# Optimization experiments

Measured on AMD Instinct MI355X. Metric: run time of the kernel, lower is better.

## Reference

```python
import jax, jax.numpy as jnp
import numpy as np

INPUT_SIZE = 300
HIDDEN = 16


def setup_inputs() -> dict:
    key = jax.random.key(0)
    ks = jax.random.split(key, 9)
    T, B = 512, 512
    s_ih = 1.0 / np.sqrt(HIDDEN)
    inp = {
        "x": jax.random.normal(ks[0], (T, B, INPUT_SIZE), dtype=jnp.float32),
        # LSTMCell params (torch gate order: i, f, g, o)
        "W_ih": jax.random.uniform(ks[1], (4 * HIDDEN, INPUT_SIZE), jnp.float32, -s_ih, s_ih),
        "W_hh": jax.random.uniform(ks[2], (4 * HIDDEN, HIDDEN), jnp.float32, -s_ih, s_ih),
        "b_ih": jax.random.uniform(ks[3], (4 * HIDDEN,), jnp.float32, -s_ih, s_ih),
        "b_hh": jax.random.uniform(ks[4], (4 * HIDDEN,), jnp.float32, -s_ih, s_ih),
        # MLP head
        "W1": jax.random.uniform(ks[5], (64, HIDDEN), jnp.float32, -s_ih, s_ih),
        "b1": jax.random.uniform(ks[6], (64,), jnp.float32, -s_ih, s_ih),
        "W2": jax.random.uniform(ks[7], (1, 64), jnp.float32, -0.125, 0.125),
        "b2": jax.random.uniform(ks[8], (1,), jnp.float32, -0.125, 0.125),
    }
    return inp


def _lstm_final_h(x, W_ih, W_hh, b_ih, b_hh):
    B = x.shape[1]
    h0 = jnp.zeros((B, HIDDEN), dtype=x.dtype)
    c0 = jnp.zeros((B, HIDDEN), dtype=x.dtype)
    # precompute input projections for all timesteps: [T, B, 4H]
    xg = jnp.einsum("tbi,gi->tbg", x, W_ih) + b_ih + b_hh

    def step(carry, xg_t):
        h, c = carry
        gates = xg_t + h @ W_hh.T  # [B, 4H]
        i, f, g, o = jnp.split(gates, 4, axis=-1)
        c = jax.nn.sigmoid(f) * c + jax.nn.sigmoid(i) * jnp.tanh(g)
        h = jax.nn.sigmoid(o) * jnp.tanh(c)
        return (h, c), None

    (h, _), _ = jax.lax.scan(step, (h0, c0), xg)
    return h  # [B, HIDDEN]


def reference(x, W_ih, W_hh, b_ih, b_hh, W1, b1, W2, b2):
    h = _lstm_final_h(x, W_ih, W_hh, b_ih, b_hh)
    # eval mode: dropout is identity
    z = jax.nn.relu(h @ W1.T + b1)
    out = 4.0 * jax.nn.sigmoid(z @ W2.T + b2)
    return out.squeeze(-1)  # [B]
```

## Files before the change

kernel.cpp:

```cpp
#include <hip/hip_runtime.h>
#include <hip/hip_bf16.h>


#define T_STEPS 512
#define BATCH   512
#define K_IN    300
#define NG      64
#define HID     16
#define DPF     8

typedef float  f32x2  __attribute__((ext_vector_type(2)));
typedef float  f32x4  __attribute__((ext_vector_type(4)));
typedef float  f32x8  __attribute__((ext_vector_type(8)));
typedef __bf16 bf16x8 __attribute__((ext_vector_type(8)));

static __device__ __forceinline__ bf16x8 cvt8(float4 lo, float4 hi) {
    f32x8 t;
    t[0] = lo.x; t[1] = lo.y; t[2] = lo.z; t[3] = lo.w;
    t[4] = hi.x; t[5] = hi.y; t[6] = hi.z; t[7] = hi.w;
    return __builtin_convertvector(t, bf16x8);
}

__global__ __launch_bounds__(256) void xg_gemm(
    const float* __restrict__ x,
    const float* __restrict__ W,
    const float* __restrict__ b_ih,
    const float* __restrict__ b_hh,
    float* __restrict__ xg)
{
    __shared__ __align__(16) __bf16 Wl[40 * 512];

    const int lane = threadIdx.x & 63;
    const int wv   = threadIdx.x >> 6;
    const int m16  = lane & 15;
    const int quad = lane >> 4;
    const int row0 = blockIdx.x * 64 + wv * 16;
    const float4 z4 = {0.f, 0.f, 0.f, 0.f};

    const float* xr = x + (size_t)(row0 + m16) * K_IN;

    float4 alo[10], ahi[10];
#pragma unroll
    for (int ks = 0; ks < 10; ++ks) {
        const int k = ks * 32 + quad * 8;
        alo[ks] = (k + 3 < K_IN) ? *(const float4*)(xr + k)     : z4;
        ahi[ks] = (k + 7 < K_IN) ? *(const float4*)(xr + k + 4) : z4;
    }

    {
        const float* wrow = W + (size_t)(wv * 16 + m16) * K_IN;
#pragma unroll
        for (int ks = 0; ks < 10; ++ks) {
            const int k = ks * 32 + quad * 8;
            const float4 lo = (k + 3 < K_IN) ? *(const float4*)(wrow + k)     : z4;
            const float4 hi = (k + 7 < K_IN) ? *(const float4*)(wrow + k + 4) : z4;
            *(bf16x8*)&Wl[(ks * 4 + wv) * 512 + lane * 8] = cvt8(lo, hi);
        }
    }
    __syncthreads();

    f32x4 acc[4];
#pragma unroll
    for (int nt = 0; nt < 4; ++nt) acc[nt] = (f32x4){0.f, 0.f, 0.f, 0.f};

#pragma unroll
    for (int ks = 0; ks < 10; ++ks) {
        const bf16x8 af = cvt8(alo[ks], ahi[ks]);
#pragma unroll
        for (int nt = 0; nt < 4; ++nt) {
            const bf16x8 bf = *(const bf16x8*)&Wl[(ks * 4 + nt) * 512 + lane * 8];
            acc[nt] = __builtin_amdgcn_mfma_f32_16x16x32_bf16(af, bf, acc[nt], 0, 0, 0);
        }
    }

    float bias[4];
#pragma unroll
    for (int nt = 0; nt < 4; ++nt)
        bias[nt] = b_ih[nt * 16 + m16] + b_hh[nt * 16 + m16];

#pragma unroll
    for (int reg = 0; reg < 4; ++reg) {
        const int R = row0 + quad * 4 + reg;
        const int t = R >> 9;
        const int b = R & (BATCH - 1);
        float4 o;
        o.x = acc[0][reg] + bias[0];
        o.y = acc[1][reg] + bias[1];
        o.z = acc[2][reg] + bias[2];
        o.w = acc[3][reg] + bias[3];
        *(float4*)(xg + ((size_t)b * T_STEPS + t) * NG + m16 * 4) = o;
    }
}

__global__ __launch_bounds__(64) void lstm_scan(
    const float* __restrict__ xg,
    const float* __restrict__ Whh,
    const float* __restrict__ W1,
    const float* __restrict__ b1,
    const float* __restrict__ W2,
    const float* __restrict__ b2,
    float* __restrict__ out)
{
    const int lane = threadIdx.x;
    const int q = lane >> 4;
    const int j = lane & 15;
    const int batch = blockIdx.x * 4 + q;
    const int pbase = (lane & 48) << 2;

    f32x2 wi2[8], wf2[8], wg2[8], wo2[8];
#pragma unroll
    for (int k4 = 0; k4 < 4; ++k4) {
        float4 a;
        a = *(const float4*)(Whh + (j     ) * HID + k4 * 4);
        wi2[k4 * 2] = (f32x2){a.x, a.y}; wi2[k4 * 2 + 1] = (f32x2){a.z, a.w};
        a = *(const float4*)(Whh + (j + 16) * HID + k4 * 4);
        wf2[k4 * 2] = (f32x2){a.x, a.y}; wf2[k4 * 2 + 1] = (f32x2){a.z, a.w};
        a = *(const float4*)(Whh + (j + 32) * HID + k4 * 4);
        wg2[k4 * 2] = (f32x2){a.x, a.y}; wg2[k4 * 2 + 1] = (f32x2){a.z, a.w};
        a = *(const float4*)(Whh + (j + 48) * HID + k4 * 4);
        wo2[k4 * 2] = (f32x2){a.x, a.y}; wo2[k4 * 2 + 1] = (f32x2){a.z, a.w};
    }

    float c = 0.f;
    f32x2 hb2[8];
#pragma unroll
    for (int k = 0; k < 8; ++k) hb2[k] = (f32x2){0.f, 0.f};

    const float* xgb = xg + (size_t)batch * T_STEPS * NG + j * 4;

    float4 ring[DPF];
#pragma unroll
    for (int u = 0; u < DPF; ++u)
        ring[u] = *(const float4*)(xgb + (size_t)u * NG);

#pragma unroll 1
    for (int tt = 0; tt < T_STEPS; tt += DPF) {
#pragma unroll
        for (int u = 0; u < DPF; ++u) {
            const int t = tt + u;
            const float4 v = ring[u];
            int tl = t + DPF; if (tl > T_STEPS - 1) tl = T_STEPS - 1;
            ring[u] = *(const float4*)(xgb + (size_t)tl * NG);

            f32x2 si2 = (f32x2){v.x, 0.f};
            f32x2 sf2 = (f32x2){v.y, 0.f};
            f32x2 sg2 = (f32x2){v.z, 0.f};
            f32x2 so2 = (f32x2){v.w, 0.f};
#pragma unroll
            for (int k = 0; k < 8; ++k) {
                si2 += wi2[k] * hb2[k];
                sf2 += wf2[k] * hb2[k];
                sg2 += wg2[k] * hb2[k];
                so2 += wo2[k] * hb2[k];
            }
            const float si = si2[0] + si2[1];
            const float sf = sf2[0] + sf2[1];
            const float sg = sg2[0] + sg2[1];
            const float so = so2[0] + so2[1];

            const float ai = __builtin_amdgcn_rcpf(1.f + __expf(-si));
            const float af = __builtin_amdgcn_rcpf(1.f + __expf(-sf));
            const float ao = __builtin_amdgcn_rcpf(1.f + __expf(-so));
            const float tg = fmaf(2.f, __builtin_amdgcn_rcpf(1.f + __expf(-2.f * sg)), -1.f);

            c = fmaf(af, c, ai * tg);
            const float th = fmaf(2.f, __builtin_amdgcn_rcpf(1.f + __expf(-2.f * c)), -1.f);
            const float h = ao * th;

            const int hI = __float_as_int(h);
#pragma unroll
            for (int k = 0; k < HID; ++k)
                hb2[k >> 1][k & 1] =
                    __int_as_float(__builtin_amdgcn_ds_bpermute(pbase + 4 * k, hI));
        }
    }

    float y = 0.f;
#pragma unroll
    for (int u4 = 0; u4 < 4; ++u4) {
        const int u = u4 * 16 + j;
        float z = b1[u];
#pragma unroll
        for (int k = 0; k < HID; ++k)
            z = fmaf(W1[u * HID + k], hb2[k >> 1][k & 1], z);
        z = fmaxf(z, 0.f);
        y = fmaf(z, W2[u], y);
    }
#pragma unroll
    for (int m = 8; m; m >>= 1) y += __shfl_xor(y, m, 64);

    if (j == 0)
        out[batch] = 4.f * __builtin_amdgcn_rcpf(1.f + __expf(-(y + b2[0])));
}

extern "C" void kernel_launch(void* const* d_in, const int* in_sizes, int n_in,
                              void* d_out, int out_size, void* d_ws, size_t ws_size,
                              hipStream_t stream) {
    const float* x    = (const float*)d_in[0];
    const float* W_ih = (const float*)d_in[1];
    const float* W_hh = (const float*)d_in[2];
    const float* b_ih = (const float*)d_in[3];
    const float* b_hh = (const float*)d_in[4];
    const float* W1   = (const float*)d_in[5];
    const float* b1   = (const float*)d_in[6];
    const float* W2   = (const float*)d_in[7];
    const float* b2   = (const float*)d_in[8];
    float* out = (float*)d_out;
    float* xg  = (float*)d_ws;

    xg_gemm<<<dim3(T_STEPS * BATCH / 64), dim3(256), 0, stream>>>(x, W_ih, b_ih, b_hh, xg);
    lstm_scan<<<dim3(BATCH / 4), dim3(64), 0, stream>>>(xg, W_hh, W1, b1, W2, b2, out);
}
```

Before: 566.5 us.

## Map one batch per wavefront with one gate per lane in LSTM scan

```diff
diff --git a/kernel.cpp b/kernel.cpp
--- a/kernel.cpp
+++ b/kernel.cpp
@@ -7,9 +7,8 @@
 #define K_IN    300
 #define NG      64
 #define HID     16
-#define DPF     8
-
-typedef float  f32x2  __attribute__((ext_vector_type(2)));
+#define CHUNK   16
+
 typedef float  f32x4  __attribute__((ext_vector_type(4)));
 typedef float  f32x8  __attribute__((ext_vector_type(8)));
 typedef __bf16 bf16x8 __attribute__((ext_vector_type(8)));
@@ -101,95 +100,105 @@
     const float* __restrict__ b2,
     float* __restrict__ out)
 {
-    const int lane = threadIdx.x;
-    const int q = lane >> 4;
-    const int j = lane & 15;
-    const int batch = blockIdx.x * 4 + q;
-    const int pbase = (lane & 48) << 2;
-
-    f32x2 wi2[8], wf2[8], wg2[8], wo2[8];
-#pragma unroll
-    for (int k4 = 0; k4 < 4; ++k4) {
-        float4 a;
-        a = *(const float4*)(Whh + (j     ) * HID + k4 * 4);
-        wi2[k4 * 2] = (f32x2){a.x, a.y}; wi2[k4 * 2 + 1] = (f32x2){a.z, a.w};
-        a = *(const float4*)(Whh + (j + 16) * HID + k4 * 4);
-        wf2[k4 * 2] = (f32x2){a.x, a.y}; wf2[k4 * 2 + 1] = (f32x2){a.z, a.w};
-        a = *(const float4*)(Whh + (j + 32) * HID + k4 * 4);
-        wg2[k4 * 2] = (f32x2){a.x, a.y}; wg2[k4 * 2 + 1] = (f32x2){a.z, a.w};
-        a = *(const float4*)(Whh + (j + 48) * HID + k4 * 4);
-        wo2[k4 * 2] = (f32x2){a.x, a.y}; wo2[k4 * 2 + 1] = (f32x2){a.z, a.w};
-    }
+    __shared__ __align__(16) float xs[2][CHUNK][NG];
+
+    const int lane  = threadIdx.x;
+    const int j     = lane & 15;
+    const int qd    = lane >> 4;
+    const int batch = blockIdx.x;
+    const int perm  = j * 4 + qd;
+
+    float w[HID];
+#pragma unroll
+    for (int k = 0; k < HID; k += 4)
+        *(float4*)&w[k] = *(const float4*)(Whh + lane * HID + k);
+
+    const float kk = (qd == 2) ? -2.f : -1.f;
+    const float mm = (qd == 2) ?  2.f :  1.f;
+    const float nn = (qd == 2) ? -1.f :  0.f;
+
+    const int aI = 4 * j, aF = 4 * (16 + j), aG = 4 * (32 + j), aO = 4 * (48 + j);
+
+    const float* xb = xg + (size_t)batch * T_STEPS * NG;
+
+#pragma unroll
+    for (int q = 0; q < 4; ++q)
+        *(float4*)((float*)xs + q * 256 + lane * 4) =
+            *(const float4*)(xb + q * 256 + lane * 4);
 
     float c = 0.f;
-    f32x2 hb2[8];
-#pragma unroll
-    for (int k = 0; k < 8; ++k) hb2[k] = (f32x2){0.f, 0.f};
-
-    const float* xgb = xg + (size_t)batch * T_STEPS * NG + j * 4;
-
-    float4 ring[DPF];
-#pragma unroll
-    for (int u = 0; u < DPF; ++u)
-        ring[u] = *(const float4*)(xgb + (size_t)u * NG);
+    float hs[HID];
+#pragma unroll
+    for (int k = 0; k < HID; ++k) hs[k] = 0.f;
 
 #pragma unroll 1
-    for (int tt = 0; tt < T_STEPS; tt += DPF) {
-#pragma unroll
-        for (int u = 0; u < DPF; ++u) {
-            const int t = tt + u;
-            const float4 v = ring[u];
-            int tl = t + DPF; if (tl > T_STEPS - 1) tl = T_STEPS - 1;
-            ring[u] = *(const float4*)(xgb + (size_t)tl * NG);
-
-            f32x2 si2 = (f32x2){v.x, 0.f};
-            f32x2 sf2 = (f32x2){v.y, 0.f};
-            f32x2 sg2 = (f32x2){v.z, 0.f};
-            f32x2 so2 = (f32x2){v.w, 0.f};
-#pragma unroll
-            for (int k = 0; k < 8; ++k) {
-                si2 += wi2[k] * hb2[k];
-                sf2 += wf2[k] * hb2[k];
-                sg2 += wg2[k] * hb2[k];
-                so2 += wo2[k] * hb2[k];
+    for (int ci = 0; ci < T_STEPS / CHUNK; ++ci) {
+        const int cur = ci & 1;
+
+        float4 nx0, nx1, nx2, nx3;
+        if (ci < T_STEPS / CHUNK - 1) {
+            const float* src = xb + (size_t)(ci + 1) * CHUNK * NG;
+            nx0 = *(const float4*)(src +   0 + lane * 4);
+            nx1 = *(const float4*)(src + 256 + lane * 4);
+            nx2 = *(const float4*)(src + 512 + lane * 4);
+            nx3 = *(const float4*)(src + 768 + lane * 4);
+        }
+
+        const float* bp = (const float*)xs + cur * (CHUNK * NG) + perm;
+
+#pragma unroll
+        for (int tin = 0; tin < CHUNK; ++tin) {
+            const float pre = bp[tin * NG];
+
+            float p0 = pre, p1 = 0.f, p2 = 0.f, p3 = 0.f;
+#pragma unroll
+            for (int k = 0; k < 4; ++k) {
+                p0 = fmaf(w[k],      hs[k],      p0);
+                p1 = fmaf(w[k + 4],  hs[k + 4],  p1);
+                p2 = fmaf(w[k + 8],  hs[k + 8],  p2);
+                p3 = fmaf(w[k + 12], hs[k + 12], p3);
             }
-            const float si = si2[0] + si2[1];
-            const float sf = sf2[0] + sf2[1];
-            const float sg = sg2[0] + sg2[1];
-            const float so = so2[0] + so2[1];
-
-            const float ai = __builtin_amdgcn_rcpf(1.f + __expf(-si));
-            const float af = __builtin_amdgcn_rcpf(1.f + __expf(-sf));
-            const float ao = __builtin_amdgcn_rcpf(1.f + __expf(-so));
-            const float tg = fmaf(2.f, __builtin_amdgcn_rcpf(1.f + __expf(-2.f * sg)), -1.f);
-
-            c = fmaf(af, c, ai * tg);
+            const float s = (p0 + p1) + (p2 + p3);
+
+            const float a   = __builtin_amdgcn_rcpf(1.f + __expf(kk * s));
+            const float act = fmaf(a, mm, nn);
+
+            const int av = __float_as_int(act);
+            const float ai = __int_as_float(__builtin_amdgcn_ds_bpermute(aI, av));
+            const float af = __int_as_float(__builtin_amdgcn_ds_bpermute(aF, av));
+            const float ag = __int_as_float(__builtin_amdgcn_ds_bpermute(aG, av));
+            const float ao = __int_as_float(__builtin_amdgcn_ds_bpermute(aO, av));
+
+            c = fmaf(af, c, ai * ag);
             const float th = fmaf(2.f, __builtin_amdgcn_rcpf(1.f + __expf(-2.f * c)), -1.f);
-            const float h = ao * th;
+            const float h  = ao * th;
 
             const int hI = __float_as_int(h);
 #pragma unroll
             for (int k = 0; k < HID; ++k)
-                hb2[k >> 1][k & 1] =
-                    __int_as_float(__builtin_amdgcn_ds_bpermute(pbase + 4 * k, hI));
-        }
-    }
-
-    float y = 0.f;
-#pragma unroll
-    for (int u4 = 0; u4 < 4; ++u4) {
-        const int u = u4 * 16 + j;
-        float z = b1[u];
-#pragma unroll
-        for (int k = 0; k < HID; ++k)
-            z = fmaf(W1[u * HID + k], hb2[k >> 1][k & 1], z);
-        z = fmaxf(z, 0.f);
-        y = fmaf(z, W2[u], y);
-    }
-#pragma unroll
-    for (int m = 8; m; m >>= 1) y += __shfl_xor(y, m, 64);
-
-    if (j == 0)
+                hs[k] = __int_as_float(__builtin_amdgcn_readlane(hI, k));
+        }
+
+        if (ci < T_STEPS / CHUNK - 1) {
+            float* wp = (float*)xs + (cur ^ 1) * (CHUNK * NG) + lane * 4;
+            *(float4*)(wp +   0) = nx0;
+            *(float4*)(wp + 256) = nx1;
+            *(float4*)(wp + 512) = nx2;
+            *(float4*)(wp + 768) = nx3;
+        }
+    }
+
+    float z = b1[lane];
+#pragma unroll
+    for (int k = 0; k < HID; ++k)
+        z = fmaf(W1[lane * HID + k], hs[k], z);
+    z = fmaxf(z, 0.f);
+    float y = z * W2[lane];
+
+#pragma unroll
+    for (int m = 1; m < 64; m <<= 1) y += __shfl_xor(y, m, 64);
+
+    if (lane == 0)
         out[batch] = 4.f * __builtin_amdgcn_rcpf(1.f + __expf(-(y + b2[0])));
 }
 
@@ -209,5 +218,5 @@
     float* xg  = (float*)d_ws;
 
     xg_gemm<<<dim3(T_STEPS * BATCH / 64), dim3(256), 0, stream>>>(x, W_ih, b_ih, b_hh, xg);
-    lstm_scan<<<dim3(BATCH / 4), dim3(64), 0, stream>>>(xg, W_hh, W1, b1, W2, b2, out);
-}
+    lstm_scan<<<dim3(BATCH), dim3(64), 0, stream>>>(xg, W_hh, W1, b1, W2, b2, out);
+}
```

New measurement: 529.2 us. 1.07x faster.
